# Kernel tuning notes

Measured on AMD Instinct MI355X. Metric: run time of the kernel, lower is better.

The kernel has to match this reference:

```python
import jax, jax.numpy as jnp
import numpy as np

ALPHA = 0.2


def setup_inputs() -> dict:
    key = jax.random.key(0)
    k1, k2, k3, k4, k5 = jax.random.split(key, 5)
    B, T, I, H, A = 256, 2048, 128, 256, 8
    x = jax.random.normal(k1, (B, T, I), dtype=jnp.float32)
    hx = jnp.zeros((1, B, H), dtype=jnp.float32)
    # weights initialized per init_weights() conventions
    W_ih = jax.random.normal(k2, (H, I), dtype=jnp.float32) * (1.0 / I ** 0.5)
    W_hh = jax.random.normal(k3, (H, H), dtype=jnp.float32) * (1.5 / H ** 0.5)
    W_actor = jax.random.normal(k4, (A, H), dtype=jnp.float32) * (1.0 / H)
    W_critic = jax.random.normal(k5, (1, H), dtype=jnp.float32) * (1.0 / H)
    return {"x": x, "hx": hx, "W_ih": W_ih, "W_hh": W_hh,
            "W_actor": W_actor, "W_critic": W_critic}


def reference(x, hx, W_ih, W_hh, W_actor, W_critic):
    # x: [B, T, I], hx: [1, B, H]
    h0 = hx[0]  # [B, H]
    # precompute input projection for all timesteps: [T, B, H]
    xproj = jnp.einsum('bti,hi->tbh', x, W_ih)

    def step(h, xp_t):
        pre = h @ W_hh.T + xp_t
        h_new = (1.0 - ALPHA) * h + ALPHA * jax.nn.relu(pre)
        return h_new, None

    h, _ = jax.lax.scan(step, h0, xproj)
    actor_logits = h @ W_actor.T   # [B, A]
    critic_value = h @ W_critic.T  # [B, 1]
    new_hx = h[None]               # [1, B, H]
    return actor_logits, critic_value, new_hx
```

## Files before the change

kernel.cpp:

```cpp
#include <hip/hip_runtime.h>
#include <hip/hip_bf16.h>
#include <stdint.h>

#define BB 256
#define TT 2048
#define II 128
#define HH 256
#define XPLD 260

typedef _Float16       f16x8     __attribute__((ext_vector_type(8)));
typedef float          f32x4     __attribute__((ext_vector_type(4)));
typedef unsigned short ushort8_t __attribute__((ext_vector_type(8)));
typedef float          float4_t  __attribute__((ext_vector_type(4)));

__device__ __forceinline__ float bf2f(unsigned short u) {
    union { unsigned int i; float f; } v; v.i = ((unsigned int)u) << 16; return v.f;
}

__global__ __launch_bounds__(512, 2)
void rnn_mfma_row2(const void* __restrict__ xv,  const void* __restrict__ hxv,
                   const void* __restrict__ Wihv, const void* __restrict__ Whhv,
                   const void* __restrict__ Wactv, const void* __restrict__ Wcritv,
                   void* __restrict__ outv)
{
    const int b    = blockIdx.x;
    const int tid  = threadIdx.x;
    const int w    = tid >> 6;
    const int l    = tid & 63;
    const int quad = l >> 4;
    const int col  = l & 15;
    const int tsel = (l >> 4) & 1;
    const int jown = w * 32 + (l & 31);
    const int aoff = ((l & 3) == 1) ? 256 : 0;

    __shared__ __align__(16) _Float16 s_h[2][512];
    __shared__ __align__(16) float    s_xp[2][16 * XPLD];
    __shared__ float s_hf[HH];
    __shared__ int s_flag;

    if (tid == 0) {
        const unsigned short* p = (const unsigned short*)Whhv;
        int cnt = 0;
        for (int i = 0; i < 256; ++i) { int e = (p[i] >> 7) & 0xFF; cnt += (e > 128) ? 1 : 0; }
        s_flag = (cnt > 16) ? 1 : 0;
    }
    __syncthreads();
    const bool f32io = (s_flag != 0);

    f16x8 bfrag[24];
#pragma unroll
    for (int c = 0; c < 12; ++c) {
#pragma unroll
        for (int t = 0; t < 2; ++t) {
            const int j  = w * 32 + t * 16 + col;
            const int k0 = 32 * c + quad * 8;
            f16x8 bv;
            if (!f32io) {
                const unsigned short* src = (k0 < HH)
                    ? ((const unsigned short*)Whhv + j * HH + k0)
                    : ((const unsigned short*)Wihv + j * II + (k0 - HH));
                ushort8_t u = *(const ushort8_t*)src;
#pragma unroll
                for (int e = 0; e < 8; ++e) bv[e] = (_Float16)bf2f(u[e]);
            } else {
                const float* src = (k0 < HH)
                    ? ((const float*)Whhv + j * HH + k0)
                    : ((const float*)Wihv + j * II + (k0 - HH));
#pragma unroll
                for (int e = 0; e < 8; ++e) bv[e] = (_Float16)src[e];
            }
            bfrag[c * 2 + t] = bv;
        }
    }

    const f32x4 kz = {0.f, 0.f, 0.f, 0.f};

    ushort8_t xru[4];
    float4_t  xrf[8];
    f16x8     xaf[4];

    auto xload = [&](int tbase) {
        if (!f32io) {
            const unsigned short* gp = (const unsigned short*)xv
                + ((size_t)b * TT + tbase + col) * II + quad * 8;
#pragma unroll
            for (int c = 0; c < 4; ++c) xru[c] = *(const ushort8_t*)(gp + 32 * c);
        } else {
            const float* gp = (const float*)xv
                + ((size_t)b * TT + tbase + col) * II + quad * 8;
#pragma unroll
            for (int c = 0; c < 4; ++c) {
                xrf[2 * c]     = *(const float4_t*)(gp + 32 * c);
                xrf[2 * c + 1] = *(const float4_t*)(gp + 32 * c + 4);
            }
        }
    };
    auto xcvt = [&]() {
        if (!f32io) {
#pragma unroll
            for (int c = 0; c < 4; ++c)
#pragma unroll
                for (int e = 0; e < 8; ++e) xaf[c][e] = (_Float16)bf2f(xru[c][e]);
        } else {
#pragma unroll
            for (int c = 0; c < 4; ++c)
#pragma unroll
                for (int e = 0; e < 8; ++e) xaf[c][e] = (_Float16)xrf[2 * c + (e >> 2)][e & 3];
        }
    };
    auto xmm = [&](float* dst) {
        f32x4 xa[2];
        xa[0] = kz; xa[1] = kz;
#pragma unroll
        for (int c = 0; c < 4; ++c)
#pragma unroll
            for (int tt = 0; tt < 2; ++tt)
                xa[tt] = __builtin_amdgcn_mfma_f32_16x16x32_f16(xaf[c], bfrag[(8 + c) * 2 + tt], xa[tt], 0, 0, 0);
#pragma unroll
        for (int tt = 0; tt < 2; ++tt)
#pragma unroll
            for (int r = 0; r < 4; ++r)
                dst[(quad * 4 + r) * XPLD + w * 32 + tt * 16 + col] = xa[tt][r];
    };

    float hreg;
    {
        if (!f32io) hreg = bf2f(((const unsigned short*)hxv)[b * HH + jown]);
        else        hreg = ((const float*)hxv)[b * HH + jown];
        _Float16 hi = (_Float16)hreg;
        _Float16 lo = (_Float16)((hreg - (float)hi) * 2048.f);
        s_h[0][jown]       = hi;
        s_h[0][256 + jown] = lo;
    }

    xload(0); xcvt(); xmm(&s_xp[0][0]);
    __syncthreads();

    for (int t = 0; t < TT; ++t) {
        const int par   = t & 1;
        const int slot  = (t >> 4) & 1;
        const int slice = t & 15;
        const int tn    = (t & ~15) + 16;
        const bool prep = (tn < TT);

        if (slice == 0 && prep) xload(tn);

        const float xp = s_xp[slot][slice * XPLD + jown];

        const _Float16* hb = s_h[par];

        if (slice == 4 && prep) xcvt();
        if (slice == 8 && prep) xmm(&s_xp[slot ^ 1][0]);

        f32x4 acc0, acc1;
        {
            f16x8 a = *(const f16x8*)(hb + aoff + quad * 8);
            acc0 = __builtin_amdgcn_mfma_f32_16x16x32_f16(a, bfrag[0], kz, 0, 0, 0);
            acc1 = __builtin_amdgcn_mfma_f32_16x16x32_f16(a, bfrag[1], kz, 0, 0, 0);
        }
#pragma unroll
        for (int c = 1; c < 8; ++c) {
            f16x8 a = *(const f16x8*)(hb + aoff + 32 * c + quad * 8);
            acc0 = __builtin_amdgcn_mfma_f32_16x16x32_f16(a, bfrag[c * 2 + 0], acc0, 0, 0, 0);
            acc1 = __builtin_amdgcn_mfma_f32_16x16x32_f16(a, bfrag[c * 2 + 1], acc1, 0, 0, 0);
        }

        float ph = tsel ? acc1[0] : acc0[0];
        float pl = tsel ? acc1[1] : acc0[1];
        float pre = (ph + xp) + pl * (1.f / 2048.f);

        hreg = 0.8f * hreg + 0.2f * fmaxf(pre, 0.f);

        _Float16 hi = (_Float16)hreg;
        _Float16 lo = (_Float16)((hreg - (float)hi) * 2048.f);
        s_h[par ^ 1][jown]       = hi;
        s_h[par ^ 1][256 + jown] = lo;

        if (t == TT - 1) s_hf[jown] = hreg;
        __syncthreads();
    }

    if (l < 32) {
        if (!f32io) ((__hip_bfloat16*)outv)[2304 + b * HH + jown] = __float2bfloat16(hreg);
        else        ((float*)outv)[2304 + b * HH + jown] = hreg;
    }

    if (tid < 9) {
        float acc = 0.f;
        if (!f32io) {
            const unsigned short* wr = (tid < 8) ? ((const unsigned short*)Wactv + tid * HH)
                                                 : (const unsigned short*)Wcritv;
            for (int i = 0; i < HH; ++i) acc += bf2f(wr[i]) * s_hf[i];
        } else {
            const float* wr = (tid < 8) ? ((const float*)Wactv + tid * HH)
                                        : (const float*)Wcritv;
            for (int i = 0; i < HH; ++i) acc += wr[i] * s_hf[i];
        }
        const int idx = (tid < 8) ? (b * 8 + tid) : (2048 + b);
        if (!f32io) ((__hip_bfloat16*)outv)[idx] = __float2bfloat16(acc);
        else        ((float*)outv)[idx] = acc;
    }
}

extern "C" void kernel_launch(void* const* d_in, const int* in_sizes, int n_in,
                              void* d_out, int out_size, void* d_ws, size_t ws_size,
                              hipStream_t stream) {
    rnn_mfma_row2<<<dim3(BB), dim3(512), 0, stream>>>(
        d_in[0], d_in[1], d_in[2], d_in[3], d_in[4], d_in[5], d_out);
}
```

Before: 1.597 ms.

## Split recurrent MFMA chain into two accumulators and trim per-step LDS writes

Splits the 8-deep dependent MFMA accumulation per step into two independent 4-deep chains that are summed at the end, shortening the serial latency on the recurrence critical path. The hi/lo halves of h are now written by separate half-waves (one store per lane instead of two), and the lo half is offset by 288 halves to change LDS bank mapping. The plain __syncthreads is replaced with an explicit lgkmcnt wait plus s_barrier and a sched_barrier. It costs extra accumulator registers and changes the summation order slightly.

```diff
diff --git a/kernel.cpp b/kernel.cpp
--- a/kernel.cpp
+++ b/kernel.cpp
@@ -7,6 +7,7 @@
 #define II 128
 #define HH 256
 #define XPLD 260
+#define LOFF 288
 
 typedef _Float16       f16x8     __attribute__((ext_vector_type(8)));
 typedef float          f32x4     __attribute__((ext_vector_type(4)));
@@ -18,10 +19,10 @@
 }
 
 __global__ __launch_bounds__(512, 2)
-void rnn_mfma_row2(const void* __restrict__ xv,  const void* __restrict__ hxv,
-                   const void* __restrict__ Wihv, const void* __restrict__ Whhv,
-                   const void* __restrict__ Wactv, const void* __restrict__ Wcritv,
-                   void* __restrict__ outv)
+void rnn_mfma_r5(const void* __restrict__ xv,  const void* __restrict__ hxv,
+                 const void* __restrict__ Wihv, const void* __restrict__ Whhv,
+                 const void* __restrict__ Wactv, const void* __restrict__ Wcritv,
+                 void* __restrict__ outv)
 {
     const int b    = blockIdx.x;
     const int tid  = threadIdx.x;
@@ -31,9 +32,10 @@
     const int col  = l & 15;
     const int tsel = (l >> 4) & 1;
     const int jown = w * 32 + (l & 31);
-    const int aoff = ((l & 3) == 1) ? 256 : 0;
-
-    __shared__ __align__(16) _Float16 s_h[2][512];
+    const int aoff = ((l & 3) == 1) ? LOFF : 0;
+    const int woff = ((l < 32) ? 0 : LOFF) + jown;
+
+    __shared__ __align__(16) _Float16 s_h[2][2 * LOFF];
     __shared__ __align__(16) float    s_xp[2][16 * XPLD];
     __shared__ float s_hf[HH];
     __shared__ int s_flag;
@@ -129,8 +131,8 @@
         else        hreg = ((const float*)hxv)[b * HH + jown];
         _Float16 hi = (_Float16)hreg;
         _Float16 lo = (_Float16)((hreg - (float)hi) * 2048.f);
-        s_h[0][jown]       = hi;
-        s_h[0][256 + jown] = lo;
+        s_h[0][jown]        = hi;
+        s_h[0][LOFF + jown] = lo;
     }
 
     xload(0); xcvt(); xmm(&s_xp[0][0]);
@@ -152,32 +154,46 @@
         if (slice == 4 && prep) xcvt();
         if (slice == 8 && prep) xmm(&s_xp[slot ^ 1][0]);
 
-        f32x4 acc0, acc1;
+        f32x4 acc0a, acc1a, acc0b, acc1b;
         {
             f16x8 a = *(const f16x8*)(hb + aoff + quad * 8);
-            acc0 = __builtin_amdgcn_mfma_f32_16x16x32_f16(a, bfrag[0], kz, 0, 0, 0);
-            acc1 = __builtin_amdgcn_mfma_f32_16x16x32_f16(a, bfrag[1], kz, 0, 0, 0);
-        }
-#pragma unroll
-        for (int c = 1; c < 8; ++c) {
+            acc0a = __builtin_amdgcn_mfma_f32_16x16x32_f16(a, bfrag[0], kz, 0, 0, 0);
+            acc1a = __builtin_amdgcn_mfma_f32_16x16x32_f16(a, bfrag[1], kz, 0, 0, 0);
+        }
+        {
+            f16x8 a = *(const f16x8*)(hb + aoff + 32 * 4 + quad * 8);
+            acc0b = __builtin_amdgcn_mfma_f32_16x16x32_f16(a, bfrag[8], kz, 0, 0, 0);
+            acc1b = __builtin_amdgcn_mfma_f32_16x16x32_f16(a, bfrag[9], kz, 0, 0, 0);
+        }
+#pragma unroll
+        for (int c = 1; c < 4; ++c) {
             f16x8 a = *(const f16x8*)(hb + aoff + 32 * c + quad * 8);
-            acc0 = __builtin_amdgcn_mfma_f32_16x16x32_f16(a, bfrag[c * 2 + 0], acc0, 0, 0, 0);
-            acc1 = __builtin_amdgcn_mfma_f32_16x16x32_f16(a, bfrag[c * 2 + 1], acc1, 0, 0, 0);
-        }
-
-        float ph = tsel ? acc1[0] : acc0[0];
-        float pl = tsel ? acc1[1] : acc0[1];
+            acc0a = __builtin_amdgcn_mfma_f32_16x16x32_f16(a, bfrag[c * 2 + 0], acc0a, 0, 0, 0);
+            acc1a = __builtin_amdgcn_mfma_f32_16x16x32_f16(a, bfrag[c * 2 + 1], acc1a, 0, 0, 0);
+            f16x8 a2 = *(const f16x8*)(hb + aoff + 32 * (c + 4) + quad * 8);
+            acc0b = __builtin_amdgcn_mfma_f32_16x16x32_f16(a2, bfrag[(c + 4) * 2 + 0], acc0b, 0, 0, 0);
+            acc1b = __builtin_amdgcn_mfma_f32_16x16x32_f16(a2, bfrag[(c + 4) * 2 + 1], acc1b, 0, 0, 0);
+        }
+
+        float pha = tsel ? acc1a[0] : acc0a[0];
+        float phb = tsel ? acc1b[0] : acc0b[0];
+        float pla = tsel ? acc1a[1] : acc0a[1];
+        float plb = tsel ? acc1b[1] : acc0b[1];
+        float ph = pha + phb;
+        float pl = pla + plb;
         float pre = (ph + xp) + pl * (1.f / 2048.f);
 
         hreg = 0.8f * hreg + 0.2f * fmaxf(pre, 0.f);
 
         _Float16 hi = (_Float16)hreg;
         _Float16 lo = (_Float16)((hreg - (float)hi) * 2048.f);
-        s_h[par ^ 1][jown]       = hi;
-        s_h[par ^ 1][256 + jown] = lo;
+        s_h[par ^ 1][woff] = (l < 32) ? hi : lo;
 
         if (t == TT - 1) s_hf[jown] = hreg;
-        __syncthreads();
+
+        asm volatile("s_waitcnt lgkmcnt(0)" ::: "memory");
+        __builtin_amdgcn_s_barrier();
+        __builtin_amdgcn_sched_barrier(0);
     }
 
     if (l < 32) {
@@ -205,6 +221,6 @@
 extern "C" void kernel_launch(void* const* d_in, const int* in_sizes, int n_in,
                               void* d_out, int out_size, void* d_ws, size_t ws_size,
                               hipStream_t stream) {
-    rnn_mfma_row2<<<dim3(BB), dim3(512), 0, stream>>>(
+    rnn_mfma_r5<<<dim3(BB), dim3(512), 0, stream>>>(
         d_in[0], d_in[1], d_in[2], d_in[3], d_in[4], d_in[5], d_out);
 }
```

Measured after the change: 1.565 ms. 1.02x faster.
